# Kernel optimization log

Measured on AMD Instinct MI355X. Metric: run time of the kernel, lower is better.

The kernel has to match this reference:

```python
import jax, jax.numpy as jnp
import numpy as np

N_PAPER, N_AUTHOR, N_INST = 500000, 300000, 10000
D = 128
E_CITES = E_WRITES = E_REV = 2000000
E_AFF = 500000


def _sage(x_src, x_dst, src, dst, Wl, bl, Wr):
    """PyG SAGEConv (mean aggr): lin_l(mean_{j->i} x_j) + lin_r(x_i).
    lin_l has bias, lin_r does not. Isolated dst nodes get zero mean."""
    n_dst = x_dst.shape[0]
    msg_sum = jax.ops.segment_sum(x_src[src], dst, num_segments=n_dst)  # [n_dst, D]
    cnt = jax.ops.segment_sum(jnp.ones(src.shape, x_src.dtype), dst, num_segments=n_dst)
    mean = msg_sum / jnp.maximum(cnt, 1.0)[:, None]
    return mean @ Wl + bl + x_dst @ Wr


def setup_inputs() -> dict:
    key = jax.random.key(0)
    ks = jax.random.split(key, 24)
    s = 1.0 / np.sqrt(D)
    inp = {
        'x_paper': jax.random.normal(ks[0], (N_PAPER, D), jnp.float32),
        'x_author': jax.random.normal(ks[1], (N_AUTHOR, D), jnp.float32),
        'x_inst': jax.random.normal(ks[2], (N_INST, D), jnp.float32),
        'cites_src': jax.random.randint(ks[3], (E_CITES,), 0, N_PAPER, jnp.int32),
        'cites_dst': jax.random.randint(ks[4], (E_CITES,), 0, N_PAPER, jnp.int32),
        'writes_src': jax.random.randint(ks[5], (E_WRITES,), 0, N_AUTHOR, jnp.int32),
        'writes_dst': jax.random.randint(ks[6], (E_WRITES,), 0, N_PAPER, jnp.int32),
        'rev_src': jax.random.randint(ks[7], (E_REV,), 0, N_PAPER, jnp.int32),
        'rev_dst': jax.random.randint(ks[8], (E_REV,), 0, N_AUTHOR, jnp.int32),
        'aff_src': jax.random.randint(ks[9], (E_AFF,), 0, N_AUTHOR, jnp.int32),
        'aff_dst': jax.random.randint(ks[10], (E_AFF,), 0, N_INST, jnp.int32),
    }
    names = ['cites', 'writes', 'rev', 'aff']
    for i, name in enumerate(names):
        kw = jax.random.split(ks[11 + i], 3)
        inp[f'Wl_{name}'] = jax.random.normal(kw[0], (D, D), jnp.float32) * s
        inp[f'bl_{name}'] = jnp.zeros((D,), jnp.float32)
        inp[f'Wr_{name}'] = jax.random.normal(kw[1], (D, D), jnp.float32) * s
    return inp


def reference(x_paper, x_author, x_inst,
              cites_src, cites_dst, writes_src, writes_dst,
              rev_src, rev_dst, aff_src, aff_dst,
              Wl_cites, bl_cites, Wr_cites,
              Wl_writes, bl_writes, Wr_writes,
              Wl_rev, bl_rev, Wr_rev,
              Wl_aff, bl_aff, Wr_aff):
    # HeteroConv sums per-relation SAGEConv outputs sharing a dst node type,
    # then the layer applies activation (relu) per node type. Dropout=0 (eval).
    h_paper = jax.nn.relu(
        _sage(x_paper, x_paper, cites_src, cites_dst, Wl_cites, bl_cites, Wr_cites)
        + _sage(x_author, x_paper, writes_src, writes_dst, Wl_writes, bl_writes, Wr_writes))
    h_author = jax.nn.relu(
        _sage(x_paper, x_author, rev_src, rev_dst, Wl_rev, bl_rev, Wr_rev))
    h_inst = jax.nn.relu(
        _sage(x_author, x_inst, aff_src, aff_dst, Wl_aff, bl_aff, Wr_aff))
    return h_paper, h_author, h_inst
```

## Files before the change

### kernel.cpp

```cpp
#include <hip/hip_runtime.h>

#define N_PAPER  500000
#define N_AUTHOR 300000
#define N_INST   10000
#define E_CITES  2000000
#define E_WRITES 2000000
#define E_REV    2000000
#define E_AFF    500000
#define E_TOT    (E_CITES + E_WRITES + E_REV + E_AFF)

#define SLOT_CITES  0
#define SLOT_WRITES (N_PAPER)
#define SLOT_REV    (2 * N_PAPER)
#define SLOT_AFF    (2 * N_PAPER + N_AUTHOR)
#define NSLOT       (2 * N_PAPER + N_AUTHOR + N_INST)

typedef short  bf16x8 __attribute__((ext_vector_type(8)));
typedef float  f32x4  __attribute__((ext_vector_type(4)));

__device__ __forceinline__ unsigned short f2b(float f) {
    unsigned int u = __float_as_uint(f);
    unsigned int r = (u + 0x7FFFu + ((u >> 16) & 1u)) >> 16;
    return (unsigned short)r;
}
__device__ __forceinline__ float b2f(unsigned short h) {
    return __uint_as_float(((unsigned int)h) << 16);
}

__global__ void count_edges(const int* __restrict__ cd, const int* __restrict__ wd,
                            const int* __restrict__ rd, const int* __restrict__ ad,
                            int* __restrict__ cnt) {
    int t = blockIdx.x * 256 + threadIdx.x;
    if (t >= E_TOT) return;
    int slot;
    if (t < E_CITES)                          slot = SLOT_CITES  + cd[t];
    else if (t < E_CITES + E_WRITES)          slot = SLOT_WRITES + wd[t - E_CITES];
    else if (t < E_CITES + E_WRITES + E_REV)  slot = SLOT_REV    + rd[t - (E_CITES + E_WRITES)];
    else                                      slot = SLOT_AFF    + ad[t - (E_CITES + E_WRITES + E_REV)];
    atomicAdd(&cnt[slot], 1);
}

__global__ void alloc_csr(const int* __restrict__ cnt, int* __restrict__ start,
                          int* __restrict__ cursor, int* __restrict__ pool) {
    int i = blockIdx.x * 256 + threadIdx.x;
    int deg = (i < NSLOT) ? cnt[i] : 0;
    int incl = deg;
    #pragma unroll
    for (int d = 1; d < 64; d <<= 1) {
        int v = __shfl_up(incl, d);
        if ((threadIdx.x & 63) >= d) incl += v;
    }
    int total = __shfl(incl, 63);
    int base = 0;
    if ((threadIdx.x & 63) == 63) base = atomicAdd(pool, total);
    base = __shfl(base, 63);
    if (i < NSLOT) {
        int s = base + incl - deg;
        start[i]  = s;
        cursor[i] = s;
    }
}

__global__ void fill_csr(const int* __restrict__ cs, const int* __restrict__ cd,
                         const int* __restrict__ wsrc, const int* __restrict__ wd,
                         const int* __restrict__ rs, const int* __restrict__ rd,
                         const int* __restrict__ asrc, const int* __restrict__ ad,
                         int* __restrict__ cursor, int* __restrict__ esrc) {
    int t = blockIdx.x * 256 + threadIdx.x;
    if (t >= E_TOT) return;
    int src, slot;
    if (t < E_CITES)                         { src = cs[t];                              slot = SLOT_CITES  + cd[t]; }
    else if (t < E_CITES + E_WRITES)         { int u = t - E_CITES;                      src = wsrc[u]; slot = SLOT_WRITES + wd[u]; }
    else if (t < E_CITES + E_WRITES + E_REV) { int u = t - (E_CITES + E_WRITES);         src = rs[u];   slot = SLOT_REV    + rd[u]; }
    else                                     { int u = t - (E_CITES + E_WRITES + E_REV); src = asrc[u]; slot = SLOT_AFF    + ad[u]; }
    int pos = atomicAdd(&cursor[slot], 1);
    esrc[pos] = src;
}

__device__ __forceinline__ int frag_idx(int k, int col) {
    return (((k >> 5) * 4 + ((k >> 3) & 3)) * 128 + col) * 8 + (k & 7);
}

__global__ void wprep(const float* __restrict__ Wl_c, const float* __restrict__ bl_c, const float* __restrict__ Wr_c,
                      const float* __restrict__ Wl_w, const float* __restrict__ bl_w, const float* __restrict__ Wr_w,
                      const float* __restrict__ Wl_r, const float* __restrict__ bl_r, const float* __restrict__ Wr_r,
                      const float* __restrict__ Wl_a, const float* __restrict__ bl_a, const float* __restrict__ Wr_a,
                      unsigned short* __restrict__ Wp_hi, unsigned short* __restrict__ Wp_lo,
                      unsigned short* __restrict__ Wa_hi, unsigned short* __restrict__ Wa_lo,
                      unsigned short* __restrict__ Wi_hi, unsigned short* __restrict__ Wi_lo,
                      float* __restrict__ bp, float* __restrict__ ba, float* __restrict__ bi) {
    int t = blockIdx.x * 256 + threadIdx.x;
    if (t < 384 * 128) {
        int k = t >> 7, j = t & 127;
        float v;
        if (k < 128)      v = Wl_c[t];
        else if (k < 256) v = Wl_w[(k - 128) * 128 + j];
        else              v = Wr_c[(k - 256) * 128 + j] + Wr_w[(k - 256) * 128 + j];
        unsigned short hi = f2b(v);
        unsigned short lo = f2b(v - b2f(hi));
        int idx = frag_idx(k, j);
        Wp_hi[idx] = hi; Wp_lo[idx] = lo;
    }
    if (t < 256 * 128) {
        int k = t >> 7, j = t & 127;
        float va = (k < 128) ? Wl_r[t] : Wr_r[(k - 128) * 128 + j];
        float vi = (k < 128) ? Wl_a[t] : Wr_a[(k - 128) * 128 + j];
        int idx = frag_idx(k, j);
        unsigned short ha = f2b(va); Wa_hi[idx] = ha; Wa_lo[idx] = f2b(va - b2f(ha));
        unsigned short hx = f2b(vi); Wi_hi[idx] = hx; Wi_lo[idx] = f2b(vi - b2f(hx));
    }
    if (t < 128) {
        bp[t] = bl_c[t] + bl_w[t];
        ba[t] = bl_r[t];
        bi[t] = bl_a[t];
    }
}

template <int NREL>
__global__ __launch_bounds__(256) void sage_mfma(
        const float* __restrict__ xdst,
        const float* __restrict__ xs0, const float* __restrict__ xs1,
        int slotbase0, int slotbase1,
        const int* __restrict__ cnt, const int* __restrict__ start,
        const int* __restrict__ esrc,
        const unsigned short* __restrict__ Wf_hi, const unsigned short* __restrict__ Wf_lo,
        const float* __restrict__ bias,
        float* __restrict__ out, int nrows) {
    constexpr int K  = (NREL + 1) * 128;
    constexpr int K2 = K * 2;
    constexpr int KB = K / 32;
    __shared__ unsigned short lds_hi[32 * K];
    __shared__ unsigned short lds_lo[32 * K];
    char* chi = (char*)lds_hi;
    char* clo = (char*)lds_lo;

    const int tid  = threadIdx.x;
    const int w    = tid >> 6;
    const int lane = tid & 63;

    for (int i = 0; i < 8; ++i) {
        const int tr   = w * 8 + i;
        const int row  = blockIdx.x * 32 + tr;
        const int swz  = (tr & 7) << 4;
        const int kbyte = lane * 4;
        if (row < nrows) {
            #pragma unroll
            for (int rel = 0; rel < NREL; ++rel) {
                const float* xs = (rel == 0) ? xs0 : xs1;
                const int slot  = (rel == 0 ? slotbase0 : slotbase1) + row;
                const int c = cnt[slot], s = start[slot];
                float a0 = 0.f, a1 = 0.f;
                int e = 0;
                for (; e + 4 <= c; e += 4) {
                    int j0 = esrc[s + e], j1 = esrc[s + e + 1];
                    int j2 = esrc[s + e + 2], j3 = esrc[s + e + 3];
                    float2 v0 = *(const float2*)(xs + (size_t)j0 * 128 + lane * 2);
                    float2 v1 = *(const float2*)(xs + (size_t)j1 * 128 + lane * 2);
                    float2 v2 = *(const float2*)(xs + (size_t)j2 * 128 + lane * 2);
                    float2 v3 = *(const float2*)(xs + (size_t)j3 * 128 + lane * 2);
                    a0 += (v0.x + v1.x) + (v2.x + v3.x);
                    a1 += (v0.y + v1.y) + (v2.y + v3.y);
                }
                for (; e < c; ++e) {
                    int j = esrc[s + e];
                    float2 v = *(const float2*)(xs + (size_t)j * 128 + lane * 2);
                    a0 += v.x; a1 += v.y;
                }
                const float sc = 1.0f / (float)(c > 0 ? c : 1);
                a0 *= sc; a1 *= sc;
                unsigned short h0 = f2b(a0), h1 = f2b(a1);
                float l0 = a0 - b2f(h0), l1 = a1 - b2f(h1);
                int off = (tr * K2 + rel * 256 + kbyte) ^ swz;
                *(unsigned int*)(chi + off) = (unsigned int)h0 | ((unsigned int)h1 << 16);
                *(unsigned int*)(clo + off) = (unsigned int)f2b(l0) | ((unsigned int)f2b(l1) << 16);
            }
            {
                float2 v = *(const float2*)(xdst + (size_t)row * 128 + lane * 2);
                unsigned short h0 = f2b(v.x), h1 = f2b(v.y);
                float l0 = v.x - b2f(h0), l1 = v.y - b2f(h1);
                int off = (tr * K2 + NREL * 256 + kbyte) ^ swz;
                *(unsigned int*)(chi + off) = (unsigned int)h0 | ((unsigned int)h1 << 16);
                *(unsigned int*)(clo + off) = (unsigned int)f2b(l0) | ((unsigned int)f2b(l1) << 16);
            }
        } else {
            #pragma unroll
            for (int rel = 0; rel <= NREL; ++rel) {
                int off = (tr * K2 + rel * 256 + kbyte) ^ swz;
                *(unsigned int*)(chi + off) = 0u;
                *(unsigned int*)(clo + off) = 0u;
            }
        }
    }
    __syncthreads();

    const int l15 = lane & 15;
    const int lg  = lane >> 4;
    const int colbase = w * 32 + l15;
    const int aswz = (l15 & 7) << 4;

    f32x4 acc00 = {0.f, 0.f, 0.f, 0.f};
    f32x4 acc01 = {0.f, 0.f, 0.f, 0.f};
    f32x4 acc10 = {0.f, 0.f, 0.f, 0.f};
    f32x4 acc11 = {0.f, 0.f, 0.f, 0.f};

    for (int kb = 0; kb < KB; ++kb) {
        const int ab  = kb * 64 + lg * 16;
        const int o0  = ((l15)      * K2 + ab) ^ aswz;
        const int o1  = ((l15 + 16) * K2 + ab) ^ aswz;
        bf16x8 a0h = *(const bf16x8*)(chi + o0);
        bf16x8 a1h = *(const bf16x8*)(chi + o1);
        bf16x8 a0l = *(const bf16x8*)(clo + o0);
        bf16x8 a1l = *(const bf16x8*)(clo + o1);

        const size_t g0 = ((size_t)(kb * 4 + lg) * 128 + colbase) * 8;
        const size_t g1 = g0 + 16 * 8;
        bf16x8 w0h = *(const bf16x8*)(Wf_hi + g0);
        bf16x8 w1h = *(const bf16x8*)(Wf_hi + g1);
        bf16x8 w0l = *(const bf16x8*)(Wf_lo + g0);
        bf16x8 w1l = *(const bf16x8*)(Wf_lo + g1);

        acc00 = __builtin_amdgcn_mfma_f32_16x16x32_bf16(a0h, w0h, acc00, 0, 0, 0);
        acc00 = __builtin_amdgcn_mfma_f32_16x16x32_bf16(a0l, w0h, acc00, 0, 0, 0);
        acc00 = __builtin_amdgcn_mfma_f32_16x16x32_bf16(a0h, w0l, acc00, 0, 0, 0);

        acc01 = __builtin_amdgcn_mfma_f32_16x16x32_bf16(a0h, w1h, acc01, 0, 0, 0);
        acc01 = __builtin_amdgcn_mfma_f32_16x16x32_bf16(a0l, w1h, acc01, 0, 0, 0);
        acc01 = __builtin_amdgcn_mfma_f32_16x16x32_bf16(a0h, w1l, acc01, 0, 0, 0);

        acc10 = __builtin_amdgcn_mfma_f32_16x16x32_bf16(a1h, w0h, acc10, 0, 0, 0);
        acc10 = __builtin_amdgcn_mfma_f32_16x16x32_bf16(a1l, w0h, acc10, 0, 0, 0);
        acc10 = __builtin_amdgcn_mfma_f32_16x16x32_bf16(a1h, w0l, acc10, 0, 0, 0);

        acc11 = __builtin_amdgcn_mfma_f32_16x16x32_bf16(a1h, w1h, acc11, 0, 0, 0);
        acc11 = __builtin_amdgcn_mfma_f32_16x16x32_bf16(a1l, w1h, acc11, 0, 0, 0);
        acc11 = __builtin_amdgcn_mfma_f32_16x16x32_bf16(a1h, w1l, acc11, 0, 0, 0);
    }

    const float b0 = bias[colbase];
    const float b1 = bias[colbase + 16];
    const int row0 = blockIdx.x * 32 + lg * 4;
    #pragma unroll
    for (int j = 0; j < 4; ++j) {
        int r = row0 + j;
        if (r < nrows) {
            out[(size_t)r * 128 + colbase]      = fmaxf(acc00[j] + b0, 0.f);
            out[(size_t)r * 128 + colbase + 16] = fmaxf(acc01[j] + b1, 0.f);
        }
        int r2 = r + 16;
        if (r2 < nrows) {
            out[(size_t)r2 * 128 + colbase]      = fmaxf(acc10[j] + b0, 0.f);
            out[(size_t)r2 * 128 + colbase + 16] = fmaxf(acc11[j] + b1, 0.f);
        }
    }
}

extern "C" void kernel_launch(void* const* d_in, const int* in_sizes, int n_in,
                              void* d_out, int out_size, void* d_ws, size_t ws_size,
                              hipStream_t stream) {
    const float* x_paper  = (const float*)d_in[0];
    const float* x_author = (const float*)d_in[1];
    const float* x_inst   = (const float*)d_in[2];
    const int* cites_src  = (const int*)d_in[3];
    const int* cites_dst  = (const int*)d_in[4];
    const int* writes_src = (const int*)d_in[5];
    const int* writes_dst = (const int*)d_in[6];
    const int* rev_src    = (const int*)d_in[7];
    const int* rev_dst    = (const int*)d_in[8];
    const int* aff_src    = (const int*)d_in[9];
    const int* aff_dst    = (const int*)d_in[10];
    const float* Wl_c = (const float*)d_in[11];
    const float* bl_c = (const float*)d_in[12];
    const float* Wr_c = (const float*)d_in[13];
    const float* Wl_w = (const float*)d_in[14];
    const float* bl_w = (const float*)d_in[15];
    const float* Wr_w = (const float*)d_in[16];
    const float* Wl_r = (const float*)d_in[17];
    const float* bl_r = (const float*)d_in[18];
    const float* Wr_r = (const float*)d_in[19];
    const float* Wl_a = (const float*)d_in[20];
    const float* bl_a = (const float*)d_in[21];
    const float* Wr_a = (const float*)d_in[22];

    float* out = (float*)d_out;

    char* ws = (char*)d_ws;
    size_t off = 0;
    int* cnt    = (int*)(ws + off); off += (size_t)NSLOT * 4;
    int* pool   = (int*)(ws + off); off += 32;
    int* start  = (int*)(ws + off); off += (size_t)NSLOT * 4;
    int* cursor = (int*)(ws + off); off += (size_t)NSLOT * 4;
    int* esrc   = (int*)(ws + off); off += (size_t)E_TOT * 4;
    unsigned short* Wp_hi = (unsigned short*)(ws + off); off += 384 * 128 * 2;
    unsigned short* Wp_lo = (unsigned short*)(ws + off); off += 384 * 128 * 2;
    unsigned short* Wa_hi = (unsigned short*)(ws + off); off += 256 * 128 * 2;
    unsigned short* Wa_lo = (unsigned short*)(ws + off); off += 256 * 128 * 2;
    unsigned short* Wi_hi = (unsigned short*)(ws + off); off += 256 * 128 * 2;
    unsigned short* Wi_lo = (unsigned short*)(ws + off); off += 256 * 128 * 2;
    float* bp   = (float*)(ws + off); off += 512;
    float* ba   = (float*)(ws + off); off += 512;
    float* bi   = (float*)(ws + off); off += 512;
    (void)ws_size; (void)out_size; (void)n_in; (void)in_sizes;

    hipMemsetAsync(ws, 0, (size_t)NSLOT * 4 + 32, stream);

    const int eblocks = (E_TOT + 255) / 256;
    count_edges<<<eblocks, 256, 0, stream>>>(cites_dst, writes_dst, rev_dst, aff_dst, cnt);
    alloc_csr<<<(NSLOT + 255) / 256, 256, 0, stream>>>(cnt, start, cursor, pool);
    fill_csr<<<eblocks, 256, 0, stream>>>(cites_src, cites_dst, writes_src, writes_dst,
                                          rev_src, rev_dst, aff_src, aff_dst, cursor, esrc);
    wprep<<<(384 * 128 + 255) / 256, 256, 0, stream>>>(
        Wl_c, bl_c, Wr_c, Wl_w, bl_w, Wr_w, Wl_r, bl_r, Wr_r, Wl_a, bl_a, Wr_a,
        Wp_hi, Wp_lo, Wa_hi, Wa_lo, Wi_hi, Wi_lo, bp, ba, bi);

    sage_mfma<2><<<(N_PAPER + 31) / 32, 256, 0, stream>>>(
        x_paper, x_paper, x_author, SLOT_CITES, SLOT_WRITES,
        cnt, start, esrc, Wp_hi, Wp_lo, bp, out, N_PAPER);
    sage_mfma<1><<<(N_AUTHOR + 31) / 32, 256, 0, stream>>>(
        x_author, x_paper, nullptr, SLOT_REV, 0,
        cnt, start, esrc, Wa_hi, Wa_lo, ba, out + (size_t)N_PAPER * 128, N_AUTHOR);
    sage_mfma<1><<<(N_INST + 31) / 32, 256, 0, stream>>>(
        x_inst, x_author, nullptr, SLOT_AFF, 0,
        cnt, start, esrc, Wi_hi, Wi_lo, bi, out + (size_t)(N_PAPER + N_AUTHOR) * 128, N_INST);
}
```

Before: 3.198 ms.

## Use 1024-thread blocks with 2 rows per wave and batched predicated gathers

Raises the block size from 256 to 1024 threads, so each of the 16 waves gathers 2 destination rows instead of 8, and each wave computes one 16x16 output tile instead of four. The neighbor gather loop now issues 8 index loads and then 8 row loads per batch, with the tail handled by clamped indices and zero-weight FMAs, which exposes more memory parallelism. The cost is some wasted loads on the tail, less MFMA reuse per wave with more W reloads from global memory, and a launch-bounds hint of (1024, 8) that may limit registers.

```diff
diff --git a/kernel.cpp b/kernel.cpp
--- a/kernel.cpp
+++ b/kernel.cpp
@@ -117,7 +117,7 @@
 }
 
 template <int NREL>
-__global__ __launch_bounds__(256) void sage_mfma(
+__global__ __launch_bounds__(1024, 8) void sage_mfma(
         const float* __restrict__ xdst,
         const float* __restrict__ xs0, const float* __restrict__ xs1,
         int slotbase0, int slotbase1,
@@ -138,10 +138,11 @@
     const int w    = tid >> 6;
     const int lane = tid & 63;
 
-    for (int i = 0; i < 8; ++i) {
-        const int tr   = w * 8 + i;
-        const int row  = blockIdx.x * 32 + tr;
-        const int swz  = (tr & 7) << 4;
+    #pragma unroll
+    for (int i = 0; i < 2; ++i) {
+        const int tr    = w * 2 + i;
+        const int row   = blockIdx.x * 32 + tr;
+        const int swz   = (tr & 7) << 4;
         const int kbyte = lane * 4;
         if (row < nrows) {
             #pragma unroll
@@ -150,21 +151,22 @@
                 const int slot  = (rel == 0 ? slotbase0 : slotbase1) + row;
                 const int c = cnt[slot], s = start[slot];
                 float a0 = 0.f, a1 = 0.f;
-                int e = 0;
-                for (; e + 4 <= c; e += 4) {
-                    int j0 = esrc[s + e], j1 = esrc[s + e + 1];
-                    int j2 = esrc[s + e + 2], j3 = esrc[s + e + 3];
-                    float2 v0 = *(const float2*)(xs + (size_t)j0 * 128 + lane * 2);
-                    float2 v1 = *(const float2*)(xs + (size_t)j1 * 128 + lane * 2);
-                    float2 v2 = *(const float2*)(xs + (size_t)j2 * 128 + lane * 2);
-                    float2 v3 = *(const float2*)(xs + (size_t)j3 * 128 + lane * 2);
-                    a0 += (v0.x + v1.x) + (v2.x + v3.x);
-                    a1 += (v0.y + v1.y) + (v2.y + v3.y);
-                }
-                for (; e < c; ++e) {
-                    int j = esrc[s + e];
-                    float2 v = *(const float2*)(xs + (size_t)j * 128 + lane * 2);
-                    a0 += v.x; a1 += v.y;
+                if (c > 0) {
+                    for (int e0 = 0; e0 < c; e0 += 8) {
+                        int jj[8];
+                        #pragma unroll
+                        for (int t = 0; t < 8; ++t) {
+                            int e = e0 + t;
+                            jj[t] = esrc[s + (e < c ? e : c - 1)];
+                        }
+                        #pragma unroll
+                        for (int t = 0; t < 8; ++t) {
+                            float2 v = *(const float2*)(xs + (size_t)jj[t] * 128 + lane * 2);
+                            float m = (e0 + t < c) ? 1.f : 0.f;
+                            a0 = fmaf(m, v.x, a0);
+                            a1 = fmaf(m, v.y, a1);
+                        }
+                    }
                 }
                 const float sc = 1.0f / (float)(c > 0 ? c : 1);
                 a0 *= sc; a1 *= sc;
@@ -195,62 +197,31 @@
 
     const int l15 = lane & 15;
     const int lg  = lane >> 4;
-    const int colbase = w * 32 + l15;
-    const int aswz = (l15 & 7) << 4;
-
-    f32x4 acc00 = {0.f, 0.f, 0.f, 0.f};
-    f32x4 acc01 = {0.f, 0.f, 0.f, 0.f};
-    f32x4 acc10 = {0.f, 0.f, 0.f, 0.f};
-    f32x4 acc11 = {0.f, 0.f, 0.f, 0.f};
-
+    const int rt  = w >> 3;
+    const int ct  = w & 7;
+    const int colbase = ct * 16 + l15;
+    const int arow = rt * 16 + l15;
+    const int aswz = (arow & 7) << 4;
+
+    f32x4 acc = {0.f, 0.f, 0.f, 0.f};
     for (int kb = 0; kb < KB; ++kb) {
-        const int ab  = kb * 64 + lg * 16;
-        const int o0  = ((l15)      * K2 + ab) ^ aswz;
-        const int o1  = ((l15 + 16) * K2 + ab) ^ aswz;
-        bf16x8 a0h = *(const bf16x8*)(chi + o0);
-        bf16x8 a1h = *(const bf16x8*)(chi + o1);
-        bf16x8 a0l = *(const bf16x8*)(clo + o0);
-        bf16x8 a1l = *(const bf16x8*)(clo + o1);
-
-        const size_t g0 = ((size_t)(kb * 4 + lg) * 128 + colbase) * 8;
-        const size_t g1 = g0 + 16 * 8;
-        bf16x8 w0h = *(const bf16x8*)(Wf_hi + g0);
-        bf16x8 w1h = *(const bf16x8*)(Wf_hi + g1);
-        bf16x8 w0l = *(const bf16x8*)(Wf_lo + g0);
-        bf16x8 w1l = *(const bf16x8*)(Wf_lo + g1);
-
-        acc00 = __builtin_amdgcn_mfma_f32_16x16x32_bf16(a0h, w0h, acc00, 0, 0, 0);
-        acc00 = __builtin_amdgcn_mfma_f32_16x16x32_bf16(a0l, w0h, acc00, 0, 0, 0);
-        acc00 = __builtin_amdgcn_mfma_f32_16x16x32_bf16(a0h, w0l, acc00, 0, 0, 0);
-
-        acc01 = __builtin_amdgcn_mfma_f32_16x16x32_bf16(a0h, w1h, acc01, 0, 0, 0);
-        acc01 = __builtin_amdgcn_mfma_f32_16x16x32_bf16(a0l, w1h, acc01, 0, 0, 0);
-        acc01 = __builtin_amdgcn_mfma_f32_16x16x32_bf16(a0h, w1l, acc01, 0, 0, 0);
-
-        acc10 = __builtin_amdgcn_mfma_f32_16x16x32_bf16(a1h, w0h, acc10, 0, 0, 0);
-        acc10 = __builtin_amdgcn_mfma_f32_16x16x32_bf16(a1l, w0h, acc10, 0, 0, 0);
-        acc10 = __builtin_amdgcn_mfma_f32_16x16x32_bf16(a1h, w0l, acc10, 0, 0, 0);
-
-        acc11 = __builtin_amdgcn_mfma_f32_16x16x32_bf16(a1h, w1h, acc11, 0, 0, 0);
-        acc11 = __builtin_amdgcn_mfma_f32_16x16x32_bf16(a1l, w1h, acc11, 0, 0, 0);
-        acc11 = __builtin_amdgcn_mfma_f32_16x16x32_bf16(a1h, w1l, acc11, 0, 0, 0);
+        const int o = (arow * K2 + kb * 64 + lg * 16) ^ aswz;
+        bf16x8 ah = *(const bf16x8*)(chi + o);
+        bf16x8 al = *(const bf16x8*)(clo + o);
+        const size_t g = ((size_t)(kb * 4 + lg) * 128 + colbase) * 8;
+        bf16x8 wh = *(const bf16x8*)(Wf_hi + g);
+        bf16x8 wl = *(const bf16x8*)(Wf_lo + g);
+        acc = __builtin_amdgcn_mfma_f32_16x16x32_bf16(ah, wh, acc, 0, 0, 0);
+        acc = __builtin_amdgcn_mfma_f32_16x16x32_bf16(al, wh, acc, 0, 0, 0);
+        acc = __builtin_amdgcn_mfma_f32_16x16x32_bf16(ah, wl, acc, 0, 0, 0);
     }
 
     const float b0 = bias[colbase];
-    const float b1 = bias[colbase + 16];
-    const int row0 = blockIdx.x * 32 + lg * 4;
+    const int row0 = blockIdx.x * 32 + rt * 16 + lg * 4;
     #pragma unroll
     for (int j = 0; j < 4; ++j) {
         int r = row0 + j;
-        if (r < nrows) {
-            out[(size_t)r * 128 + colbase]      = fmaxf(acc00[j] + b0, 0.f);
-            out[(size_t)r * 128 + colbase + 16] = fmaxf(acc01[j] + b1, 0.f);
-        }
-        int r2 = r + 16;
-        if (r2 < nrows) {
-            out[(size_t)r2 * 128 + colbase]      = fmaxf(acc10[j] + b0, 0.f);
-            out[(size_t)r2 * 128 + colbase + 16] = fmaxf(acc11[j] + b1, 0.f);
-        }
+        if (r < nrows) out[(size_t)r * 128 + colbase] = fmaxf(acc[j] + b0, 0.f);
     }
 }
 
@@ -312,13 +283,13 @@
         Wl_c, bl_c, Wr_c, Wl_w, bl_w, Wr_w, Wl_r, bl_r, Wr_r, Wl_a, bl_a, Wr_a,
         Wp_hi, Wp_lo, Wa_hi, Wa_lo, Wi_hi, Wi_lo, bp, ba, bi);
 
-    sage_mfma<2><<<(N_PAPER + 31) / 32, 256, 0, stream>>>(
+    sage_mfma<2><<<(N_PAPER + 31) / 32, 1024, 0, stream>>>(
         x_paper, x_paper, x_author, SLOT_CITES, SLOT_WRITES,
         cnt, start, esrc, Wp_hi, Wp_lo, bp, out, N_PAPER);
-    sage_mfma<1><<<(N_AUTHOR + 31) / 32, 256, 0, stream>>>(
+    sage_mfma<1><<<(N_AUTHOR + 31) / 32, 1024, 0, stream>>>(
         x_author, x_paper, nullptr, SLOT_REV, 0,
         cnt, start, esrc, Wa_hi, Wa_lo, ba, out + (size_t)N_PAPER * 128, N_AUTHOR);
-    sage_mfma<1><<<(N_INST + 31) / 32, 256, 0, stream>>>(
+    sage_mfma<1><<<(N_INST + 31) / 32, 1024, 0, stream>>>(
         x_inst, x_author, nullptr, SLOT_AFF, 0,
         cnt, start, esrc, Wi_hi, Wi_lo, bi, out + (size_t)(N_PAPER + N_AUTHOR) * 128, N_INST);
 }
```

New measurement: 2.793 ms. -12.7%, faster.
